# Optimization experiments

Hardware: AMD Instinct MI355X
Metric: run time of the kernel (lower is better)

## Reference

```python
import jax, jax.numpy as jnp
import numpy as np

B, C, N_IN = 32, 64, 10475
N_OUT = 2619
NNZ = 8 * N_OUT  # ~8 barycentric entries per output vertex


def setup_inputs() -> dict:
    key = jax.random.key(0)
    k1, k2, k3, k4 = jax.random.split(key, 4)
    x = jax.random.normal(k1, (B, C, N_IN), dtype=jnp.float32)
    # Sparse mesh-sampling operator M [N_OUT, N_IN] in COO form,
    # sparsity pattern shared across the whole batch.
    M_rows = jax.random.randint(k2, (NNZ,), 0, N_OUT, dtype=jnp.int32)
    M_cols = jax.random.randint(k3, (NNZ,), 0, N_IN, dtype=jnp.int32)
    M_vals = jax.random.uniform(k4, (NNZ,), dtype=jnp.float32)
    return {"x": x, "M_rows": M_rows, "M_cols": M_cols, "M_vals": M_vals}


def reference(x, M_rows, M_cols, M_vals):
    """Batched spmm: out[b, c, r] = sum_{k: M_rows[k]==r} M_vals[k] * x[b, c, M_cols[k]].

    Equivalent to the torch module: for each batch element, M @ x[b].T, stacked,
    then transposed back to [B, C, N_OUT]. Here the batch loop is fused into a
    single gather + segment_sum that reuses the shared sparsity pattern.
    """
    # Gather source vertex features for every nnz entry: [B, C, NNZ]
    g = x[:, :, M_cols] * M_vals
    # segment_sum reduces over the leading axis -> move nnz to front
    g = jnp.moveaxis(g, 2, 0)                                   # [NNZ, B, C]
    out = jax.ops.segment_sum(g, M_rows, num_segments=N_OUT)    # [N_OUT, B, C]
    return jnp.moveaxis(out, 0, 2)                              # [B, C, N_OUT]
```

## Files before the change

### kernel.cpp

```cpp
#include <hip/hip_runtime.h>
#include <hip/hip_fp16.h>
#include <stdint.h>

#define Bdim   32
#define Cdim   64
#define N_IN   10475
#define N_OUT  2619
#define NNZ    (8 * N_OUT)
#define MAIN_BLK 512
#define CHUNK  41
#define SMALL_BLK 256
#define Gpair  2
#define NBLK   (Bdim * Cdim / Gpair)

#define SENT_META 0x0FFF0000u

#define OFF_OFFS   10480
#define OFF_ENT    20976
#define OFF_ELAST  (OFF_ENT + 20 * MAIN_BLK * 16)
#define WS_NEEDED  (OFF_ELAST + MAIN_BLK * 8)
#define ENT_U2     ((WS_NEEDED - OFF_ENT) / 8)

static __device__ __forceinline__ uint32_t pack_h2(float a, float b) {
    __half2 h = __float22half2_rn(make_float2(a, b));
    return *(uint32_t*)&h;
}
static __device__ __forceinline__ float2 unpack_h2(uint32_t u) {
    __half2 h = *(__half2*)&u;
    return __half22float2(h);
}

__global__ __launch_bounds__(SMALL_BLK) void init_ws(
        int* __restrict__ cursor, uint2* __restrict__ ent2) {
    int i = blockIdx.x * SMALL_BLK + threadIdx.x;
    if (i < N_OUT) cursor[i] = 0;
    if (i < ENT_U2) ent2[i] = make_uint2(SENT_META, 0u);
}

__global__ __launch_bounds__(SMALL_BLK) void hist_rows(
        const int* __restrict__ rows, int* __restrict__ counts) {
    int k = blockIdx.x * SMALL_BLK + threadIdx.x;
    if (k < NNZ) atomicAdd(&counts[rows[k]], 1);
}

__global__ __launch_bounds__(1024) void scan_counts(
        int* __restrict__ counts, int* __restrict__ offsets) {
    __shared__ int wsum[16];
    const int t = threadIdx.x, lane = t & 63, w = t >> 6;
    const int base = t * 3;
    int v0 = (base + 0 < N_OUT) ? counts[base + 0] : 0;
    int v1 = (base + 1 < N_OUT) ? counts[base + 1] : 0;
    int v2 = (base + 2 < N_OUT) ? counts[base + 2] : 0;
    int s = v0 + v1 + v2;
    const int tot = s;
    #pragma unroll
    for (int d = 1; d < 64; d <<= 1) {
        int n = __shfl_up(s, d);
        if (lane >= d) s += n;
    }
    if (lane == 63) wsum[w] = s;
    __syncthreads();
    if (t < 16) {
        int ws_ = wsum[t];
        #pragma unroll
        for (int d = 1; d < 16; d <<= 1) {
            int n = __shfl_up(ws_, d);
            if (t >= d) ws_ += n;
        }
        wsum[t] = ws_;
    }
    __syncthreads();
    int excl = ((w > 0) ? wsum[w - 1] : 0) + (s - tot);
    if (base + 0 <= N_OUT) { offsets[base + 0] = excl; if (base + 0 < N_OUT) counts[base + 0] = excl; }
    excl += v0;
    if (base + 1 <= N_OUT) { offsets[base + 1] = excl; if (base + 1 < N_OUT) counts[base + 1] = excl; }
    excl += v1;
    if (base + 2 <= N_OUT) { offsets[base + 2] = excl; if (base + 2 < N_OUT) counts[base + 2] = excl; }
}

__global__ __launch_bounds__(SMALL_BLK) void scatter_entries(
        const int* __restrict__ rows, const int* __restrict__ cols,
        const float* __restrict__ vals,
        int* __restrict__ cursor, const int* __restrict__ offsets,
        uint2* __restrict__ ent2, uint2* __restrict__ entLast) {
    int k = blockIdx.x * SMALL_BLK + threadIdx.x;
    if (k < NNZ) {
        int r = rows[k];
        int p = atomicAdd(&cursor[r], 1);
        uint32_t flag = (p == offsets[r + 1] - 1) ? 0x80000000u : 0u;
        uint32_t meta = flag | ((uint32_t)r << 16) | ((uint32_t)cols[k] << 2);
        uint2 e = make_uint2(meta, __float_as_uint(vals[k]));
        int t = p / CHUNK;
        int s = p - t * CHUNK;
        if (s < 40) ent2[(s >> 1) * (MAIN_BLK * 2) + t * 2 + (s & 1)] = e;
        else        entLast[t] = e;
    }
}

__global__ __launch_bounds__(MAIN_BLK, 6) void spmm_g2h(
        const float* __restrict__ x,
        const uint4* __restrict__ ent4,
        const uint2* __restrict__ entLast,
        float* __restrict__ out) {
    __shared__ uint32_t xs[N_IN];
    __shared__ uint32_t out2[N_OUT];
    __shared__ int      wCarryRow[8];
    __shared__ float    wC0[8], wC1[8];

    const int blk  = blockIdx.x;
    const int t    = threadIdx.x, lane = t & 63, w = t >> 6;
    const float* __restrict__ xr0 = x + (size_t)(Gpair * blk) * N_IN;
    const float* __restrict__ xr1 = xr0 + N_IN;

    #pragma unroll 4
    for (int i = t; i < N_IN; i += MAIN_BLK) xs[i] = pack_h2(xr0[i], xr1[i]);
    #pragma unroll
    for (int i = t; i < N_OUT; i += MAIN_BLK) out2[i] = 0u;
    __syncthreads();

    float acc0 = 0.f, acc1 = 0.f, f0 = 0.f, f1 = 0.f;
    int firstRow = -1;

#define FEED(meta, vb) do {                                              \
        uint32_t xp = *(const uint32_t*)((const char*)xs + ((meta) & 0xFFFFu)); \
        float v = __uint_as_float(vb);                                   \
        float2 xf = unpack_h2(xp);                                       \
        acc0 = fmaf(v, xf.x, acc0);                                      \
        acc1 = fmaf(v, xf.y, acc1);                                      \
        if ((int)(meta) < 0) {                                           \
            int row_ = (int)(((meta) >> 16) & 0xFFFu);                   \
            if (firstRow < 0) { firstRow = row_; f0 = acc0; f1 = acc1; } \
            else out2[row_] = pack_h2(acc0, acc1);                       \
            acc0 = 0.f; acc1 = 0.f;                                      \
        }                                                                \
    } while (0)

    #pragma unroll
    for (int jb = 0; jb < 5; ++jb) {
        uint4 q0 = ent4[(jb * 4 + 0) * MAIN_BLK + t];
        uint4 q1 = ent4[(jb * 4 + 1) * MAIN_BLK + t];
        uint4 q2 = ent4[(jb * 4 + 2) * MAIN_BLK + t];
        uint4 q3 = ent4[(jb * 4 + 3) * MAIN_BLK + t];
        FEED(q0.x, q0.y); FEED(q0.z, q0.w);
        FEED(q1.x, q1.y); FEED(q1.z, q1.w);
        FEED(q2.x, q2.y); FEED(q2.z, q2.w);
        FEED(q3.x, q3.y); FEED(q3.z, q3.w);
    }
    uint2 el = entLast[t];
    FEED(el.x, el.y);
#undef FEED

    const int   carryRow = (int)((el.x >> 16) & 0xFFFu);
    const float c0 = acc0, c1 = acc1;

    int   pRow = __shfl_up(carryRow, 1);
    float p0   = __shfl_up(c0, 1);
    float p1   = __shfl_up(c1, 1);
    if (lane == 63) { wCarryRow[w] = carryRow; wC0[w] = c0; wC1[w] = c1; }
    __syncthreads();
    if (lane == 0) {
        pRow = (w > 0) ? wCarryRow[w - 1] : -1;
        p0   = (w > 0) ? wC0[w - 1] : 0.f;
        p1   = (w > 0) ? wC1[w - 1] : 0.f;
    }

    if (firstRow >= 0 && firstRow < N_OUT) {
        bool m = (pRow == firstRow);
        out2[firstRow] = pack_h2(f0 + (m ? p0 : 0.f), f1 + (m ? p1 : 0.f));
    }
    __syncthreads();

    float* __restrict__ o0 = out + (size_t)(Gpair * blk) * N_OUT;
    float* __restrict__ o1 = o0 + N_OUT;
    #pragma unroll
    for (int i = t; i < N_OUT; i += MAIN_BLK) {
        float2 vv = unpack_h2(out2[i]);
        o0[i] = vv.x;
        o1[i] = vv.y;
    }
}

__global__ __launch_bounds__(SMALL_BLK) void spmm_raw(
        const float* __restrict__ x,
        const int* __restrict__ rows,
        const int* __restrict__ cols,
        const float* __restrict__ vals,
        float* __restrict__ out) {
    __shared__ float x_lds[N_IN];
    __shared__ float out_lds[N_OUT];
    const int bc = blockIdx.x;
    const float* __restrict__ xrow = x + (size_t)bc * N_IN;
    for (int i = threadIdx.x; i < N_IN; i += SMALL_BLK) x_lds[i] = xrow[i];
    for (int i = threadIdx.x; i < N_OUT; i += SMALL_BLK) out_lds[i] = 0.0f;
    __syncthreads();
    for (int k = threadIdx.x; k < NNZ; k += SMALL_BLK) {
        atomicAdd(&out_lds[rows[k]], vals[k] * x_lds[cols[k]]);
    }
    __syncthreads();
    float* __restrict__ orow = out + (size_t)bc * N_OUT;
    for (int i = threadIdx.x; i < N_OUT; i += SMALL_BLK) orow[i] = out_lds[i];
}

extern "C" void kernel_launch(void* const* d_in, const int* in_sizes, int n_in,
                              void* d_out, int out_size, void* d_ws, size_t ws_size,
                              hipStream_t stream) {
    const float* x    = (const float*)d_in[0];
    const int*   rows = (const int*)d_in[1];
    const int*   cols = (const int*)d_in[2];
    const float* vals = (const float*)d_in[3];
    float*       out  = (float*)d_out;

    if (ws_size >= (size_t)WS_NEEDED) {
        char*  ws      = (char*)d_ws;
        int*   cursor  = (int*)ws;
        int*   offsets = (int*)(ws + OFF_OFFS);
        uint2* ent2    = (uint2*)(ws + OFF_ENT);
        const uint4* ent4 = (const uint4*)(ws + OFF_ENT);
        uint2* entLast = (uint2*)(ws + OFF_ELAST);

        const int gi = (ENT_U2 + SMALL_BLK - 1) / SMALL_BLK;
        const int gk = (NNZ + SMALL_BLK - 1) / SMALL_BLK;

        init_ws<<<gi, SMALL_BLK, 0, stream>>>(cursor, ent2);
        hist_rows<<<gk, SMALL_BLK, 0, stream>>>(rows, cursor);
        scan_counts<<<1, 1024, 0, stream>>>(cursor, offsets);
        scatter_entries<<<gk, SMALL_BLK, 0, stream>>>(rows, cols, vals, cursor,
                                                      offsets, ent2, entLast);
        spmm_g2h<<<NBLK, MAIN_BLK, 0, stream>>>(x, ent4, entLast, out);
    } else {
        spmm_raw<<<Bdim * Cdim, SMALL_BLK, 0, stream>>>(x, rows, cols, vals, out);
    }
}
```

Before: 157.8 us.

## Fuse CSR preprocessing into one single-block kernel using LDS histogram and scan

Replaces the four preprocessing kernels (init, global-atomic histogram, scan, scatter) with a single 1024-thread block that keeps counts and offsets in shared memory and holds the row indices in registers between passes. It also drops the full-buffer sentinel initialisation and only writes sentinels into the padding slots of the last chunk, on the basis that NNZ fills every other slot. The aim is to remove three kernel launches, their inter-kernel gaps and the global atomic traffic. In exchange, the whole preprocessing now runs serially on one CU, and correctness depends on NNZ exactly filling all chunks except the last one.

```diff
diff --git a/kernel.cpp b/kernel.cpp
--- a/kernel.cpp
+++ b/kernel.cpp
@@ -15,11 +15,9 @@
 
 #define SENT_META 0x0FFF0000u
 
-#define OFF_OFFS   10480
-#define OFF_ENT    20976
+#define OFF_ENT    0
 #define OFF_ELAST  (OFF_ENT + 20 * MAIN_BLK * 16)
 #define WS_NEEDED  (OFF_ELAST + MAIN_BLK * 8)
-#define ENT_U2     ((WS_NEEDED - OFF_ENT) / 8)
 
 static __device__ __forceinline__ uint32_t pack_h2(float a, float b) {
     __half2 h = __float22half2_rn(make_float2(a, b));
@@ -30,27 +28,39 @@
     return __half22float2(h);
 }
 
-__global__ __launch_bounds__(SMALL_BLK) void init_ws(
-        int* __restrict__ cursor, uint2* __restrict__ ent2) {
-    int i = blockIdx.x * SMALL_BLK + threadIdx.x;
-    if (i < N_OUT) cursor[i] = 0;
-    if (i < ENT_U2) ent2[i] = make_uint2(SENT_META, 0u);
-}
-
-__global__ __launch_bounds__(SMALL_BLK) void hist_rows(
-        const int* __restrict__ rows, int* __restrict__ counts) {
-    int k = blockIdx.x * SMALL_BLK + threadIdx.x;
-    if (k < NNZ) atomicAdd(&counts[rows[k]], 1);
-}
-
-__global__ __launch_bounds__(1024) void scan_counts(
-        int* __restrict__ counts, int* __restrict__ offsets) {
+#define PREP_BLK 1024
+#define PREP_ITERS 21
+
+__global__ __launch_bounds__(PREP_BLK) void prep(
+        const int* __restrict__ rows, const int* __restrict__ cols,
+        const float* __restrict__ vals,
+        uint2* __restrict__ ent2, uint2* __restrict__ entLast) {
+    __shared__ int cnt[N_OUT];
+    __shared__ int offs[N_OUT + 1];
     __shared__ int wsum[16];
     const int t = threadIdx.x, lane = t & 63, w = t >> 6;
+
+    if (t >= 1 && t <= 40) {
+        uint2 e = make_uint2(SENT_META, 0u);
+        if (t < 40) ent2[(t >> 1) * (MAIN_BLK * 2) + 511 * 2 + (t & 1)] = e;
+        else        entLast[511] = e;
+    }
+    for (int i = t; i < N_OUT; i += PREP_BLK) cnt[i] = 0;
+    __syncthreads();
+
+    int rreg[PREP_ITERS];
+    #pragma unroll
+    for (int j = 0; j < PREP_ITERS; ++j) {
+        int k = t + j * PREP_BLK;
+        rreg[j] = (k < NNZ) ? rows[k] : -1;
+        if (rreg[j] >= 0) atomicAdd(&cnt[rreg[j]], 1);
+    }
+    __syncthreads();
+
     const int base = t * 3;
-    int v0 = (base + 0 < N_OUT) ? counts[base + 0] : 0;
-    int v1 = (base + 1 < N_OUT) ? counts[base + 1] : 0;
-    int v2 = (base + 2 < N_OUT) ? counts[base + 2] : 0;
+    int v0 = (base + 0 < N_OUT) ? cnt[base + 0] : 0;
+    int v1 = (base + 1 < N_OUT) ? cnt[base + 1] : 0;
+    int v2 = (base + 2 < N_OUT) ? cnt[base + 2] : 0;
     int s = v0 + v1 + v2;
     const int tot = s;
     #pragma unroll
@@ -71,29 +81,27 @@
     }
     __syncthreads();
     int excl = ((w > 0) ? wsum[w - 1] : 0) + (s - tot);
-    if (base + 0 <= N_OUT) { offsets[base + 0] = excl; if (base + 0 < N_OUT) counts[base + 0] = excl; }
+    if (base + 0 <= N_OUT) { offs[base + 0] = excl; if (base + 0 < N_OUT) cnt[base + 0] = excl; }
     excl += v0;
-    if (base + 1 <= N_OUT) { offsets[base + 1] = excl; if (base + 1 < N_OUT) counts[base + 1] = excl; }
+    if (base + 1 <= N_OUT) { offs[base + 1] = excl; if (base + 1 < N_OUT) cnt[base + 1] = excl; }
     excl += v1;
-    if (base + 2 <= N_OUT) { offsets[base + 2] = excl; if (base + 2 < N_OUT) counts[base + 2] = excl; }
-}
-
-__global__ __launch_bounds__(SMALL_BLK) void scatter_entries(
-        const int* __restrict__ rows, const int* __restrict__ cols,
-        const float* __restrict__ vals,
-        int* __restrict__ cursor, const int* __restrict__ offsets,
-        uint2* __restrict__ ent2, uint2* __restrict__ entLast) {
-    int k = blockIdx.x * SMALL_BLK + threadIdx.x;
-    if (k < NNZ) {
-        int r = rows[k];
-        int p = atomicAdd(&cursor[r], 1);
-        uint32_t flag = (p == offsets[r + 1] - 1) ? 0x80000000u : 0u;
-        uint32_t meta = flag | ((uint32_t)r << 16) | ((uint32_t)cols[k] << 2);
-        uint2 e = make_uint2(meta, __float_as_uint(vals[k]));
-        int t = p / CHUNK;
-        int s = p - t * CHUNK;
-        if (s < 40) ent2[(s >> 1) * (MAIN_BLK * 2) + t * 2 + (s & 1)] = e;
-        else        entLast[t] = e;
+    if (base + 2 <= N_OUT) { offs[base + 2] = excl; if (base + 2 < N_OUT) cnt[base + 2] = excl; }
+    __syncthreads();
+
+    #pragma unroll
+    for (int j = 0; j < PREP_ITERS; ++j) {
+        int k = t + j * PREP_BLK;
+        if (k < NNZ) {
+            int r = rreg[j];
+            int p = atomicAdd(&cnt[r], 1);
+            uint32_t flag = (p == offs[r + 1] - 1) ? 0x80000000u : 0u;
+            uint32_t meta = flag | ((uint32_t)r << 16) | ((uint32_t)cols[k] << 2);
+            uint2 e = make_uint2(meta, __float_as_uint(vals[k]));
+            int tt = p / CHUNK;
+            int ss = p - tt * CHUNK;
+            if (ss < 40) ent2[(ss >> 1) * (MAIN_BLK * 2) + tt * 2 + (ss & 1)] = e;
+            else         entLast[tt] = e;
+        }
     }
 }
 
@@ -212,20 +220,11 @@
 
     if (ws_size >= (size_t)WS_NEEDED) {
         char*  ws      = (char*)d_ws;
-        int*   cursor  = (int*)ws;
-        int*   offsets = (int*)(ws + OFF_OFFS);
         uint2* ent2    = (uint2*)(ws + OFF_ENT);
         const uint4* ent4 = (const uint4*)(ws + OFF_ENT);
         uint2* entLast = (uint2*)(ws + OFF_ELAST);
 
-        const int gi = (ENT_U2 + SMALL_BLK - 1) / SMALL_BLK;
-        const int gk = (NNZ + SMALL_BLK - 1) / SMALL_BLK;
-
-        init_ws<<<gi, SMALL_BLK, 0, stream>>>(cursor, ent2);
-        hist_rows<<<gk, SMALL_BLK, 0, stream>>>(rows, cursor);
-        scan_counts<<<1, 1024, 0, stream>>>(cursor, offsets);
-        scatter_entries<<<gk, SMALL_BLK, 0, stream>>>(rows, cols, vals, cursor,
-                                                      offsets, ent2, entLast);
+        prep<<<1, PREP_BLK, 0, stream>>>(rows, cols, vals, ent2, entLast);
         spmm_g2h<<<NBLK, MAIN_BLK, 0, stream>>>(x, ent4, entLast, out);
     } else {
         spmm_raw<<<Bdim * Cdim, SMALL_BLK, 0, stream>>>(x, rows, cols, vals, out);
```

After: 190.9 us. 21.0% more time.
